# Kernel tuning notes

Hardware: AMD Instinct MI355X
Metric: run time of the kernel (lower is better)

## Reference

```python
import jax, jax.numpy as jnp
import numpy as np

N_NODES = 100000
N_EDGES = 3200000
IN_DIM, HID_DIM, OUT_DIM = 8, 64, 112

def _glorot(key, fan_in, fan_out):
    lim = jnp.sqrt(6.0 / (fan_in + fan_out))
    return jax.random.uniform(key, (fan_in, fan_out), jnp.float32, -lim, lim)

def setup_inputs() -> dict:
    key = jax.random.key(0)
    ks = jax.random.split(key, 8)
    x = jax.random.normal(ks[0], (N_NODES, IN_DIM), jnp.float32)
    edge_index = jax.random.randint(ks[1], (2, N_EDGES), 0, N_NODES, jnp.int64 if jax.config.read('jax_enable_x64') else jnp.int32)
    return {
        'x': x,
        'edge_index': edge_index,
        'W1': _glorot(ks[2], IN_DIM, HID_DIM),  'b1': jnp.zeros((HID_DIM,), jnp.float32),
        'W2': _glorot(ks[3], HID_DIM, HID_DIM), 'b2': jnp.zeros((HID_DIM,), jnp.float32),
        'W3': _glorot(ks[4], HID_DIM, OUT_DIM), 'b3': jnp.zeros((OUT_DIM,), jnp.float32),
    }

def _gcn_conv(x, src, dst, W, b, n):
    # PyG GCNConv: add self-loops, symmetric normalization, x @ W, scatter-add, + bias
    h = x @ W                                   # [N, F_out]
    loop = jnp.arange(n, dtype=src.dtype)
    s = jnp.concatenate([src, loop])            # source (j)
    d = jnp.concatenate([dst, loop])            # target (i)
    deg = jax.ops.segment_sum(jnp.ones_like(d, dtype=h.dtype), d, num_segments=n)
    dinv = jnp.where(deg > 0, jax.lax.rsqrt(deg), 0.0)
    norm = dinv[s] * dinv[d]                    # [E+N]
    msg = h[s] * norm[:, None]                  # gather + scale, [E+N, F_out]
    out = jax.ops.segment_sum(msg, d, num_segments=n)
    return out + b

def reference(x, edge_index, W1, b1, W2, b2, W3, b3):
    # eval mode: dropout is identity
    n = x.shape[0]
    src, dst = edge_index[0], edge_index[1]
    h = jax.nn.relu(_gcn_conv(x, src, dst, W1, b1, n))
    h = jax.nn.relu(_gcn_conv(h, src, dst, W2, b2, n))
    return _gcn_conv(h, src, dst, W3, b3, n)
```

## Files before the change

### kernel.cpp

```cpp
#include <hip/hip_runtime.h>
#include <hip/hip_fp16.h>


#define NNODES 100000
#define NEDGES 3200000
#define BW     128
#define NB     ((NNODES + BW - 1) / BW)
#define NSUB   8
#define SUBCAP 768
#define CAP    (NSUB * SUBCAP)
#define PAD    16
#define SLOTCAP 72
#define TILE   4096
#define EPT    (TILE / 256)
#define NFB    ((NEDGES + TILE - 1) / TILE)

typedef unsigned long long u64;


__global__ void bcur_init_kernel(int* __restrict__ bcur) {
    int i = blockIdx.x * blockDim.x + threadIdx.x;
    if (i < NB * NSUB) {
        int b  = i / NSUB;
        int xc = i % NSUB;
        bcur[i * PAD] = b * CAP + xc * SUBCAP;
    }
}

__global__ __launch_bounds__(256) void bfill_kernel(
        const int* __restrict__ src, const int* __restrict__ dst,
        int* __restrict__ bcur, u64* __restrict__ tmp) {
    __shared__ int cnt[NB];
    __shared__ int gbase[NB];
    int xc = blockIdx.x & (NSUB - 1);
    int e0 = blockIdx.x * TILE;

    for (int t = threadIdx.x; t < NB; t += 256) cnt[t] = 0;
    __syncthreads();

    u64 pk[EPT];
    int bb[EPT];
    int loff[EPT];
#pragma unroll
    for (int j = 0; j < EPT; ++j) {
        int e = e0 + j * 256 + threadIdx.x;
        if (e < NEDGES) {
            int d = dst[e];
            int s = src[e];
            bb[j] = d >> 7;
            pk[j] = ((u64)(unsigned)d << 32) | (unsigned)s;
            loff[j] = atomicAdd(&cnt[bb[j]], 1);
        } else {
            bb[j] = -1;
        }
    }
    __syncthreads();

    for (int b = threadIdx.x; b < NB; b += 256) {
        int c = cnt[b];
        gbase[b] = c ? atomicAdd(&bcur[(b * NSUB + xc) * PAD], c) : 0;
    }
    __syncthreads();

#pragma unroll
    for (int j = 0; j < EPT; ++j) {
        if (bb[j] >= 0) {
            int b = bb[j];
            int p = gbase[b] + loff[j];
            int sb = b * CAP + xc * SUBCAP;
            if ((unsigned)(p - sb) < (unsigned)SUBCAP)
                tmp[p] = pk[j];
        }
    }
}

__global__ void place_kernel(const u64* __restrict__ tmp, const int* __restrict__ bcur,
                             int* __restrict__ csr_src, int* __restrict__ rend,
                             float* __restrict__ dinv) {
    __shared__ int cur[BW];
    int b  = blockIdx.x;
    int lo = b * BW;

    for (int t = threadIdx.x; t < BW; t += blockDim.x)
        cur[t] = (lo + t) * SLOTCAP;
    __syncthreads();
#pragma unroll
    for (int xc = 0; xc < NSUB; ++xc) {
        int sb = b * CAP + xc * SUBCAP;
        int se = bcur[(b * NSUB + xc) * PAD];
        if (se > sb + SUBCAP) se = sb + SUBCAP;
        for (int k = sb + threadIdx.x; k < se; k += blockDim.x) {
            u64 pk = __builtin_nontemporal_load(&tmp[k]);
            int d = (int)(pk >> 32) - lo;
            int s = (int)(pk & 0xffffffffu);
            if ((unsigned)d < (unsigned)BW) {
                int pos = atomicAdd(&cur[d], 1);
                if (pos - (lo + d) * SLOTCAP < SLOTCAP)
                    csr_src[pos] = s;
            }
        }
    }
    __syncthreads();
    for (int t = threadIdx.x; t < BW; t += blockDim.x) {
        int i = lo + t;
        if (i < NNODES) {
            int deg = cur[t] - i * SLOTCAP;
            if (deg > SLOTCAP) deg = SLOTCAP;
            rend[i] = i * SLOTCAP + deg;
            dinv[i] = rsqrtf((float)deg + 1.0f);
        }
    }
}


__global__ void prescale_kernel(const float* __restrict__ x, const float* __restrict__ dinv,
                                float* __restrict__ xs) {
    int idx = blockIdx.x * blockDim.x + threadIdx.x;
    if (idx >= NNODES * 2) return;
    float di = dinv[idx >> 1];
    float4 v = ((const float4*)x)[idx];
    v.x *= di; v.y *= di; v.z *= di; v.w *= di;
    ((float4*)xs)[idx] = v;
}

#define ACC4(A, V) { A.x += V.x; A.y += V.y; A.z += V.z; A.w += V.w; }

template<int F>
__global__ void gather_kernel(const float* __restrict__ hs, const int* __restrict__ rend,
                              const int* __restrict__ csr_src, float* __restrict__ agg) {
    constexpr int NQ = F / 4;
    int idx = blockIdx.x * blockDim.x + threadIdx.x;
    if (idx >= NNODES * NQ) return;
    int i = idx / NQ;
    int q = idx % NQ;

    const float4* t4 = (const float4*)hs;
    float4 a0 = t4[i * NQ + q];
    float4 a1 = make_float4(0.f, 0.f, 0.f, 0.f), a2 = a1, a3 = a1;
    int beg = i * SLOTCAP, end = rend[i];
    int k = beg;
    for (; k + 4 <= end; k += 4) {
        int s0 = __builtin_nontemporal_load(&csr_src[k + 0]);
        int s1 = __builtin_nontemporal_load(&csr_src[k + 1]);
        int s2 = __builtin_nontemporal_load(&csr_src[k + 2]);
        int s3 = __builtin_nontemporal_load(&csr_src[k + 3]);
        float4 v0 = t4[s0 * NQ + q];
        float4 v1 = t4[s1 * NQ + q];
        float4 v2 = t4[s2 * NQ + q];
        float4 v3 = t4[s3 * NQ + q];
        ACC4(a0, v0) ACC4(a1, v1) ACC4(a2, v2) ACC4(a3, v3)
    }
    for (; k < end; ++k) {
        float4 v = t4[csr_src[k] * NQ + q];
        ACC4(a0, v)
    }
    ACC4(a0, a1) ACC4(a2, a3) ACC4(a0, a2)
    ((float4*)agg)[i * NQ + q] = a0;
}

#define H8_ACC(RAW, X0, X1) {                                            \
        const __half2* hp_ = (const __half2*)&(RAW);                     \
        float2 f0_ = __half22float2(hp_[0]);                             \
        float2 f1_ = __half22float2(hp_[1]);                             \
        float2 f2_ = __half22float2(hp_[2]);                             \
        float2 f3_ = __half22float2(hp_[3]);                             \
        X0.x += f0_.x; X0.y += f0_.y; X0.z += f1_.x; X0.w += f1_.y;      \
        X1.x += f2_.x; X1.y += f2_.y; X1.z += f3_.x; X1.w += f3_.y; }

__global__ void gather64h_kernel(const __half* __restrict__ hs, const int* __restrict__ rend,
                                 const int* __restrict__ csr_src, float* __restrict__ agg) {
    int idx = blockIdx.x * blockDim.x + threadIdx.x;
    if (idx >= NNODES * 8) return;
    int i = idx >> 3;
    int q = idx & 7;

    const float4* h4 = (const float4*)hs;
    float4 a0 = make_float4(0.f, 0.f, 0.f, 0.f), a1 = a0, b0 = a0, b1 = a0;

    float4 self = h4[(size_t)i * 8 + q];
    H8_ACC(self, a0, a1)

    int beg = i * SLOTCAP, end = rend[i];
    int k = beg;
    for (; k + 4 <= end; k += 4) {
        int s0 = __builtin_nontemporal_load(&csr_src[k + 0]);
        int s1 = __builtin_nontemporal_load(&csr_src[k + 1]);
        int s2 = __builtin_nontemporal_load(&csr_src[k + 2]);
        int s3 = __builtin_nontemporal_load(&csr_src[k + 3]);
        float4 r0 = h4[(size_t)s0 * 8 + q];
        float4 r1 = h4[(size_t)s1 * 8 + q];
        float4 r2 = h4[(size_t)s2 * 8 + q];
        float4 r3 = h4[(size_t)s3 * 8 + q];
        H8_ACC(r0, a0, a1) H8_ACC(r1, b0, b1) H8_ACC(r2, a0, a1) H8_ACC(r3, b0, b1)
    }
    for (; k < end; ++k) {
        float4 r = h4[(size_t)csr_src[k] * 8 + q];
        H8_ACC(r, a0, a1)
    }
    ACC4(a0, b0) ACC4(a1, b1)

    float4* o4 = (float4*)(agg + (size_t)i * 64 + q * 8);
    o4[0] = a0;
    o4[1] = a1;
}

template<int FIN, int FOUT, bool RELU, bool SCALE, bool OUTH>
__global__ __launch_bounds__(256) void transform_kernel(
        const float* __restrict__ agg, const float* __restrict__ dinv,
        const float* __restrict__ W, const float* __restrict__ b,
        void* __restrict__ outp) {
    __shared__ float Ws[FIN * FOUT];
    __shared__ float bs[FOUT];
    for (int t = threadIdx.x; t < FIN * FOUT; t += 256) Ws[t] = W[t];
    for (int t = threadIdx.x; t < FOUT; t += 256) bs[t] = b[t];
    __syncthreads();

    int i = blockIdx.x * 256 + threadIdx.x;
    if (i >= NNODES) return;

    const float4* row4 = (const float4*)(agg + (size_t)i * FIN);
    float di = dinv[i];

    constexpr int NC = FOUT / 16;
    for (int c = 0; c < NC; ++c) {
        float4 a0 = make_float4(0.f, 0.f, 0.f, 0.f), a1 = a0, a2 = a0, a3 = a0;
        const float* wbase = Ws + c * 16;
#define FMA16(RV, KK) { const float4* wq = (const float4*)(wbase + (KK) * FOUT);     \
        float4 w0 = wq[0], w1 = wq[1], w2 = wq[2], w3 = wq[3];                       \
        a0.x += (RV)*w0.x; a0.y += (RV)*w0.y; a0.z += (RV)*w0.z; a0.w += (RV)*w0.w;  \
        a1.x += (RV)*w1.x; a1.y += (RV)*w1.y; a1.z += (RV)*w1.z; a1.w += (RV)*w1.w;  \
        a2.x += (RV)*w2.x; a2.y += (RV)*w2.y; a2.z += (RV)*w2.z; a2.w += (RV)*w2.w;  \
        a3.x += (RV)*w3.x; a3.y += (RV)*w3.y; a3.z += (RV)*w3.z; a3.w += (RV)*w3.w; }
#pragma unroll
        for (int k4 = 0; k4 < FIN / 4; ++k4) {
            float4 rv = row4[k4];
            FMA16(rv.x, 4 * k4 + 0)
            FMA16(rv.y, 4 * k4 + 1)
            FMA16(rv.z, 4 * k4 + 2)
            FMA16(rv.w, 4 * k4 + 3)
        }
#undef FMA16
        const float4* bq = (const float4*)(bs + c * 16);
        float4 b0 = bq[0], b1 = bq[1], b2 = bq[2], b3 = bq[3];
#define POST(A, B) { A.x = A.x * di + B.x; A.y = A.y * di + B.y;                     \
        A.z = A.z * di + B.z; A.w = A.w * di + B.w;                                  \
        if (RELU) { A.x = fmaxf(A.x, 0.f); A.y = fmaxf(A.y, 0.f);                    \
                    A.z = fmaxf(A.z, 0.f); A.w = fmaxf(A.w, 0.f); }                  \
        if (SCALE) { A.x *= di; A.y *= di; A.z *= di; A.w *= di; } }
        POST(a0, b0) POST(a1, b1) POST(a2, b2) POST(a3, b3)
#undef POST
        if (OUTH) {
            __half* hout = (__half*)outp + (size_t)i * FOUT;
            union { float4 f4; __half2 h2[4]; } u0, u1;
            u0.h2[0] = __floats2half2_rn(a0.x, a0.y);
            u0.h2[1] = __floats2half2_rn(a0.z, a0.w);
            u0.h2[2] = __floats2half2_rn(a1.x, a1.y);
            u0.h2[3] = __floats2half2_rn(a1.z, a1.w);
            u1.h2[0] = __floats2half2_rn(a2.x, a2.y);
            u1.h2[1] = __floats2half2_rn(a2.z, a2.w);
            u1.h2[2] = __floats2half2_rn(a3.x, a3.y);
            u1.h2[3] = __floats2half2_rn(a3.z, a3.w);
            ((float4*)hout)[c * 2 + 0] = u0.f4;
            ((float4*)hout)[c * 2 + 1] = u1.f4;
        } else {
            float4* out4 = (float4*)((float*)outp + (size_t)i * FOUT);
            out4[c * 4 + 0] = a0;
            out4[c * 4 + 1] = a1;
            out4[c * 4 + 2] = a2;
            out4[c * 4 + 3] = a3;
        }
    }
}

extern "C" void kernel_launch(void* const* d_in, const int* in_sizes, int n_in,
                              void* d_out, int out_size, void* d_ws, size_t ws_size,
                              hipStream_t stream) {
    const float* x  = (const float*)d_in[0];
    const int*   ei = (const int*)d_in[1];
    const float* W1 = (const float*)d_in[2];
    const float* b1 = (const float*)d_in[3];
    const float* W2 = (const float*)d_in[4];
    const float* b2 = (const float*)d_in[5];
    const float* W3 = (const float*)d_in[6];
    const float* b3 = (const float*)d_in[7];

    const int* src = ei;
    const int* dst = ei + NEDGES;

    float* out = (float*)d_out;

    char* w = (char*)d_ws;
    int*   bcur    = (int*)w;                 w += NB * NSUB * PAD * 4;
    int*   rend    = (int*)w;                 w += ((NNODES + 3) / 4) * 16;
    float* dinv    = (float*)w;               w += ((NNODES + 3) / 4) * 16;
    int*   csr_src = (int*)w;                 w += (size_t)NNODES * SLOTCAP * 4;
    float* xs      = (float*)w;               w += (size_t)NNODES * 8 * 4;
    float* aggX    = (float*)w;               w += (size_t)NNODES * 8 * 4;
    char*  big     = w;                       w += (size_t)NB * CAP * 8;
    u64*    tmp   = (u64*)big;
    float*  bufG  = (float*)big;
    __half* bufHh = (__half*)(big + (size_t)NNODES * 64 * 4);

    const int B = 256;
    int gC   = (NB * NSUB + B - 1) / B;
    int gN2  = (NNODES * 2 + B - 1) / B;
    int gT   = (NNODES + 255) / 256;
    int gG8  = (NNODES * 2 + B - 1) / B;
    int gG64 = (NNODES * 8 + B - 1) / B;

    bcur_init_kernel<<<gC, B, 0, stream>>>(bcur);
    bfill_kernel <<<NFB, 256, 0, stream>>>(src, dst, bcur, tmp);
    place_kernel <<<NB, B, 0, stream>>>(tmp, bcur, csr_src, rend, dinv);

    prescale_kernel<<<gN2, B, 0, stream>>>(x, dinv, xs);
    gather_kernel<8><<<gG8, B, 0, stream>>>(xs, rend, csr_src, aggX);
    transform_kernel<8, 64, true, true, true><<<gT, 256, 0, stream>>>(aggX, dinv, W1, b1, bufHh);

    gather64h_kernel<<<gG64, B, 0, stream>>>(bufHh, rend, csr_src, bufG);
    transform_kernel<64, 64, true, true, true><<<gT, 256, 0, stream>>>(bufG, dinv, W2, b2, bufHh);

    gather64h_kernel<<<gG64, B, 0, stream>>>(bufHh, rend, csr_src, bufG);
    transform_kernel<64, 112, false, false, false><<<gT, 256, 0, stream>>>(bufG, dinv, W3, b3, out);
}
```

Baseline: 343.6 us.

## Fuse 64-wide neighbor gather with dense transform and enlarge bucket-fill tiles

```diff
diff --git a/kernel.cpp b/kernel.cpp
--- a/kernel.cpp
+++ b/kernel.cpp
@@ -11,8 +11,9 @@
 #define CAP    (NSUB * SUBCAP)
 #define PAD    16
 #define SLOTCAP 72
-#define TILE   4096
-#define EPT    (TILE / 256)
+#define BFT    512
+#define TILE   8192
+#define EPT    (TILE / BFT)
 #define NFB    ((NEDGES + TILE - 1) / TILE)
 
 typedef unsigned long long u64;
@@ -27,7 +28,7 @@
     }
 }
 
-__global__ __launch_bounds__(256) void bfill_kernel(
+__global__ __launch_bounds__(BFT) void bfill_kernel(
         const int* __restrict__ src, const int* __restrict__ dst,
         int* __restrict__ bcur, u64* __restrict__ tmp) {
     __shared__ int cnt[NB];
@@ -35,7 +36,7 @@
     int xc = blockIdx.x & (NSUB - 1);
     int e0 = blockIdx.x * TILE;
 
-    for (int t = threadIdx.x; t < NB; t += 256) cnt[t] = 0;
+    for (int t = threadIdx.x; t < NB; t += BFT) cnt[t] = 0;
     __syncthreads();
 
     u64 pk[EPT];
@@ -43,7 +44,7 @@
     int loff[EPT];
 #pragma unroll
     for (int j = 0; j < EPT; ++j) {
-        int e = e0 + j * 256 + threadIdx.x;
+        int e = e0 + j * BFT + threadIdx.x;
         if (e < NEDGES) {
             int d = dst[e];
             int s = src[e];
@@ -56,7 +57,7 @@
     }
     __syncthreads();
 
-    for (int b = threadIdx.x; b < NB; b += 256) {
+    for (int b = threadIdx.x; b < NB; b += BFT) {
         int c = cnt[b];
         gbase[b] = c ? atomicAdd(&bcur[(b * NSUB + xc) * PAD], c) : 0;
     }
@@ -158,57 +159,11 @@
     ((float4*)agg)[i * NQ + q] = a0;
 }
 
-#define H8_ACC(RAW, X0, X1) {                                            \
-        const __half2* hp_ = (const __half2*)&(RAW);                     \
-        float2 f0_ = __half22float2(hp_[0]);                             \
-        float2 f1_ = __half22float2(hp_[1]);                             \
-        float2 f2_ = __half22float2(hp_[2]);                             \
-        float2 f3_ = __half22float2(hp_[3]);                             \
-        X0.x += f0_.x; X0.y += f0_.y; X0.z += f1_.x; X0.w += f1_.y;      \
-        X1.x += f2_.x; X1.y += f2_.y; X1.z += f3_.x; X1.w += f3_.y; }
-
-__global__ void gather64h_kernel(const __half* __restrict__ hs, const int* __restrict__ rend,
-                                 const int* __restrict__ csr_src, float* __restrict__ agg) {
-    int idx = blockIdx.x * blockDim.x + threadIdx.x;
-    if (idx >= NNODES * 8) return;
-    int i = idx >> 3;
-    int q = idx & 7;
-
-    const float4* h4 = (const float4*)hs;
-    float4 a0 = make_float4(0.f, 0.f, 0.f, 0.f), a1 = a0, b0 = a0, b1 = a0;
-
-    float4 self = h4[(size_t)i * 8 + q];
-    H8_ACC(self, a0, a1)
-
-    int beg = i * SLOTCAP, end = rend[i];
-    int k = beg;
-    for (; k + 4 <= end; k += 4) {
-        int s0 = __builtin_nontemporal_load(&csr_src[k + 0]);
-        int s1 = __builtin_nontemporal_load(&csr_src[k + 1]);
-        int s2 = __builtin_nontemporal_load(&csr_src[k + 2]);
-        int s3 = __builtin_nontemporal_load(&csr_src[k + 3]);
-        float4 r0 = h4[(size_t)s0 * 8 + q];
-        float4 r1 = h4[(size_t)s1 * 8 + q];
-        float4 r2 = h4[(size_t)s2 * 8 + q];
-        float4 r3 = h4[(size_t)s3 * 8 + q];
-        H8_ACC(r0, a0, a1) H8_ACC(r1, b0, b1) H8_ACC(r2, a0, a1) H8_ACC(r3, b0, b1)
-    }
-    for (; k < end; ++k) {
-        float4 r = h4[(size_t)csr_src[k] * 8 + q];
-        H8_ACC(r, a0, a1)
-    }
-    ACC4(a0, b0) ACC4(a1, b1)
-
-    float4* o4 = (float4*)(agg + (size_t)i * 64 + q * 8);
-    o4[0] = a0;
-    o4[1] = a1;
-}
-
-template<int FIN, int FOUT, bool RELU, bool SCALE, bool OUTH>
+template<int FIN, int FOUT>
 __global__ __launch_bounds__(256) void transform_kernel(
         const float* __restrict__ agg, const float* __restrict__ dinv,
         const float* __restrict__ W, const float* __restrict__ b,
-        void* __restrict__ outp) {
+        __half* __restrict__ outp) {
     __shared__ float Ws[FIN * FOUT];
     __shared__ float bs[FOUT];
     for (int t = threadIdx.x; t < FIN * FOUT; t += 256) Ws[t] = W[t];
@@ -242,32 +197,147 @@
 #undef FMA16
         const float4* bq = (const float4*)(bs + c * 16);
         float4 b0 = bq[0], b1 = bq[1], b2 = bq[2], b3 = bq[3];
-#define POST(A, B) { A.x = A.x * di + B.x; A.y = A.y * di + B.y;                     \
-        A.z = A.z * di + B.z; A.w = A.w * di + B.w;                                  \
-        if (RELU) { A.x = fmaxf(A.x, 0.f); A.y = fmaxf(A.y, 0.f);                    \
-                    A.z = fmaxf(A.z, 0.f); A.w = fmaxf(A.w, 0.f); }                  \
-        if (SCALE) { A.x *= di; A.y *= di; A.z *= di; A.w *= di; } }
+#define POST(A, B) { A.x = fmaxf(A.x * di + B.x, 0.f) * di;                          \
+        A.y = fmaxf(A.y * di + B.y, 0.f) * di;                                       \
+        A.z = fmaxf(A.z * di + B.z, 0.f) * di;                                       \
+        A.w = fmaxf(A.w * di + B.w, 0.f) * di; }
         POST(a0, b0) POST(a1, b1) POST(a2, b2) POST(a3, b3)
 #undef POST
+        __half* hout = outp + (size_t)i * FOUT;
+        union { float4 f4; __half2 h2[4]; } u0, u1;
+        u0.h2[0] = __floats2half2_rn(a0.x, a0.y);
+        u0.h2[1] = __floats2half2_rn(a0.z, a0.w);
+        u0.h2[2] = __floats2half2_rn(a1.x, a1.y);
+        u0.h2[3] = __floats2half2_rn(a1.z, a1.w);
+        u1.h2[0] = __floats2half2_rn(a2.x, a2.y);
+        u1.h2[1] = __floats2half2_rn(a2.z, a2.w);
+        u1.h2[2] = __floats2half2_rn(a3.x, a3.y);
+        u1.h2[3] = __floats2half2_rn(a3.z, a3.w);
+        ((float4*)hout)[c * 2 + 0] = u0.f4;
+        ((float4*)hout)[c * 2 + 1] = u1.f4;
+    }
+}
+
+
+#define H8_TO(RAW, X0, X1) {                                             \
+        const __half2* hp_ = (const __half2*)&(RAW);                     \
+        float2 f0_ = __half22float2(hp_[0]);                             \
+        float2 f1_ = __half22float2(hp_[1]);                             \
+        float2 f2_ = __half22float2(hp_[2]);                             \
+        float2 f3_ = __half22float2(hp_[3]);                             \
+        X0.x += f0_.x; X0.y += f0_.y; X0.z += f1_.x; X0.w += f1_.y;      \
+        X1.x += f2_.x; X1.y += f2_.y; X1.z += f3_.x; X1.w += f3_.y; }
+
+#define ROWE(KK) ((KK & 3) == 0 ? A[KK >> 2].x : (KK & 3) == 1 ? A[KK >> 2].y \
+                 : (KK & 3) == 2 ? A[KK >> 2].z : A[KK >> 2].w)
+
+template<int FOUT, bool RELU, bool SCALE, bool OUTH>
+__global__ __launch_bounds__(256) void fused64_kernel(
+        const __half* __restrict__ hs, const int* __restrict__ rend,
+        const int* __restrict__ csr_src, const float* __restrict__ dinv,
+        const float* __restrict__ W, const float* __restrict__ b,
+        void* __restrict__ outp) {
+    constexpr int CH  = (FOUT % 32 == 0) ? 32 : 28;
+    constexpr int NCH = FOUT / CH;
+    constexpr int NQ  = CH / 4;
+    __shared__ float Ws[64 * FOUT];
+    __shared__ float bs[FOUT];
+    for (int t = threadIdx.x; t < 64 * FOUT; t += 256) Ws[t] = W[t];
+    for (int t = threadIdx.x; t < FOUT; t += 256) bs[t] = b[t];
+    __syncthreads();
+
+    int idx = blockIdx.x * 256 + threadIdx.x;
+    if (idx >= NNODES * 2) return;
+    int i = idx >> 1;
+    int h = idx & 1;
+
+    const float4* h4 = (const float4*)hs;
+    size_t qb = (size_t)i * 8 + h * 4;
+
+    float4 A[8];
+#pragma unroll
+    for (int j = 0; j < 8; ++j) A[j] = make_float4(0.f, 0.f, 0.f, 0.f);
+    {
+        float4 s0 = h4[qb + 0], s1 = h4[qb + 1], s2 = h4[qb + 2], s3 = h4[qb + 3];
+        H8_TO(s0, A[0], A[1]) H8_TO(s1, A[2], A[3])
+        H8_TO(s2, A[4], A[5]) H8_TO(s3, A[6], A[7])
+    }
+    int beg = i * SLOTCAP, end = rend[i];
+    int k = beg;
+    for (; k + 2 <= end; k += 2) {
+        int n0 = __builtin_nontemporal_load(&csr_src[k + 0]);
+        int n1 = __builtin_nontemporal_load(&csr_src[k + 1]);
+        size_t q0 = (size_t)n0 * 8 + h * 4;
+        size_t q1 = (size_t)n1 * 8 + h * 4;
+        float4 r0 = h4[q0 + 0], r1 = h4[q0 + 1], r2 = h4[q0 + 2], r3 = h4[q0 + 3];
+        float4 t0 = h4[q1 + 0], t1 = h4[q1 + 1], t2 = h4[q1 + 2], t3 = h4[q1 + 3];
+        H8_TO(r0, A[0], A[1]) H8_TO(r1, A[2], A[3])
+        H8_TO(r2, A[4], A[5]) H8_TO(r3, A[6], A[7])
+        H8_TO(t0, A[0], A[1]) H8_TO(t1, A[2], A[3])
+        H8_TO(t2, A[4], A[5]) H8_TO(t3, A[6], A[7])
+    }
+    for (; k < end; ++k) {
+        int n0 = __builtin_nontemporal_load(&csr_src[k]);
+        size_t q0 = (size_t)n0 * 8 + h * 4;
+        float4 r0 = h4[q0 + 0], r1 = h4[q0 + 1], r2 = h4[q0 + 2], r3 = h4[q0 + 3];
+        H8_TO(r0, A[0], A[1]) H8_TO(r1, A[2], A[3])
+        H8_TO(r2, A[4], A[5]) H8_TO(r3, A[6], A[7])
+    }
+
+    float di = dinv[i];
+    int kb = h * 32;
+
+    for (int c = 0; c < NCH; ++c) {
+        float4 C[NQ];
+#pragma unroll
+        for (int j = 0; j < NQ; ++j) C[j] = make_float4(0.f, 0.f, 0.f, 0.f);
+#pragma unroll
+        for (int kk = 0; kk < 32; ++kk) {
+            float rv = ROWE(kk);
+            const float4* wq = (const float4*)(Ws + (kb + kk) * FOUT + c * CH);
+#pragma unroll
+            for (int j = 0; j < NQ; ++j) {
+                C[j].x += rv * wq[j].x; C[j].y += rv * wq[j].y;
+                C[j].z += rv * wq[j].z; C[j].w += rv * wq[j].w;
+            }
+        }
+#pragma unroll
+        for (int j = 0; j < NQ; ++j) {
+            C[j].x += __shfl_xor(C[j].x, 1);
+            C[j].y += __shfl_xor(C[j].y, 1);
+            C[j].z += __shfl_xor(C[j].z, 1);
+            C[j].w += __shfl_xor(C[j].w, 1);
+        }
+        const float4* bq = (const float4*)(bs + c * CH);
+#pragma unroll
+        for (int j = 0; j < NQ; ++j) {
+            float4 bb = bq[j];
+            C[j].x = C[j].x * di + bb.x; C[j].y = C[j].y * di + bb.y;
+            C[j].z = C[j].z * di + bb.z; C[j].w = C[j].w * di + bb.w;
+            if (RELU) {
+                C[j].x = fmaxf(C[j].x, 0.f); C[j].y = fmaxf(C[j].y, 0.f);
+                C[j].z = fmaxf(C[j].z, 0.f); C[j].w = fmaxf(C[j].w, 0.f);
+            }
+            if (SCALE) { C[j].x *= di; C[j].y *= di; C[j].z *= di; C[j].w *= di; }
+        }
         if (OUTH) {
-            __half* hout = (__half*)outp + (size_t)i * FOUT;
-            union { float4 f4; __half2 h2[4]; } u0, u1;
-            u0.h2[0] = __floats2half2_rn(a0.x, a0.y);
-            u0.h2[1] = __floats2half2_rn(a0.z, a0.w);
-            u0.h2[2] = __floats2half2_rn(a1.x, a1.y);
-            u0.h2[3] = __floats2half2_rn(a1.z, a1.w);
-            u1.h2[0] = __floats2half2_rn(a2.x, a2.y);
-            u1.h2[1] = __floats2half2_rn(a2.z, a2.w);
-            u1.h2[2] = __floats2half2_rn(a3.x, a3.y);
-            u1.h2[3] = __floats2half2_rn(a3.z, a3.w);
-            ((float4*)hout)[c * 2 + 0] = u0.f4;
-            ((float4*)hout)[c * 2 + 1] = u1.f4;
+            __half* hrow = (__half*)outp + (size_t)i * FOUT + c * CH;
+#pragma unroll
+            for (int p = 0; p < NQ / 2; ++p) {
+                if ((p & 1) == h) {
+                    union { float4 f4; __half2 h2[4]; } u;
+                    u.h2[0] = __floats2half2_rn(C[2 * p].x, C[2 * p].y);
+                    u.h2[1] = __floats2half2_rn(C[2 * p].z, C[2 * p].w);
+                    u.h2[2] = __floats2half2_rn(C[2 * p + 1].x, C[2 * p + 1].y);
+                    u.h2[3] = __floats2half2_rn(C[2 * p + 1].z, C[2 * p + 1].w);
+                    ((float4*)hrow)[p] = u.f4;
+                }
+            }
         } else {
-            float4* out4 = (float4*)((float*)outp + (size_t)i * FOUT);
-            out4[c * 4 + 0] = a0;
-            out4[c * 4 + 1] = a1;
-            out4[c * 4 + 2] = a2;
-            out4[c * 4 + 3] = a3;
+            float* orow = (float*)outp + (size_t)i * FOUT + c * CH;
+#pragma unroll
+            for (int j = 0; j < NQ; ++j)
+                if ((j & 1) == h) ((float4*)orow)[j] = C[j];
         }
     }
 }
@@ -297,28 +367,28 @@
     float* xs      = (float*)w;               w += (size_t)NNODES * 8 * 4;
     float* aggX    = (float*)w;               w += (size_t)NNODES * 8 * 4;
     char*  big     = w;                       w += (size_t)NB * CAP * 8;
-    u64*    tmp   = (u64*)big;
-    float*  bufG  = (float*)big;
-    __half* bufHh = (__half*)(big + (size_t)NNODES * 64 * 4);
+    u64*    tmp    = (u64*)big;
+    __half* stateA = (__half*)big;
+    __half* stateB = (__half*)(big + (size_t)NNODES * 64 * 2);
 
     const int B = 256;
     int gC   = (NB * NSUB + B - 1) / B;
     int gN2  = (NNODES * 2 + B - 1) / B;
     int gT   = (NNODES + 255) / 256;
     int gG8  = (NNODES * 2 + B - 1) / B;
-    int gG64 = (NNODES * 8 + B - 1) / B;
+    int gF   = (NNODES * 2 + 255) / 256;
 
     bcur_init_kernel<<<gC, B, 0, stream>>>(bcur);
-    bfill_kernel <<<NFB, 256, 0, stream>>>(src, dst, bcur, tmp);
+    bfill_kernel <<<NFB, BFT, 0, stream>>>(src, dst, bcur, tmp);
     place_kernel <<<NB, B, 0, stream>>>(tmp, bcur, csr_src, rend, dinv);
 
     prescale_kernel<<<gN2, B, 0, stream>>>(x, dinv, xs);
     gather_kernel<8><<<gG8, B, 0, stream>>>(xs, rend, csr_src, aggX);
-    transform_kernel<8, 64, true, true, true><<<gT, 256, 0, stream>>>(aggX, dinv, W1, b1, bufHh);
-
-    gather64h_kernel<<<gG64, B, 0, stream>>>(bufHh, rend, csr_src, bufG);
-    transform_kernel<64, 64, true, true, true><<<gT, 256, 0, stream>>>(bufG, dinv, W2, b2, bufHh);
-
-    gather64h_kernel<<<gG64, B, 0, stream>>>(bufHh, rend, csr_src, bufG);
-    transform_kernel<64, 112, false, false, false><<<gT, 256, 0, stream>>>(bufG, dinv, W3, b3, out);
-}
+    transform_kernel<8, 64><<<gT, 256, 0, stream>>>(aggX, dinv, W1, b1, stateA);
+
+    fused64_kernel<64, true, true, true><<<gF, 256, 0, stream>>>(
+        stateA, rend, csr_src, dinv, W2, b2, stateB);
+
+    fused64_kernel<112, false, false, false><<<gF, 256, 0, stream>>>(
+        stateB, rend, csr_src, dinv, W3, b3, out);
+}
```

Result: slower. 391.6 us (+14.0%).

## Pack bucketed edges into 32-bit words and enlarge bucket-fill tiles

Applied to the files above, without the earlier changes.

```diff
diff --git a/kernel.cpp b/kernel.cpp
--- a/kernel.cpp
+++ b/kernel.cpp
@@ -11,11 +11,12 @@
 #define CAP    (NSUB * SUBCAP)
 #define PAD    16
 #define SLOTCAP 72
-#define TILE   4096
-#define EPT    (TILE / 256)
+#define BFT    512
+#define TILE   8192
+#define EPT    (TILE / BFT)
 #define NFB    ((NEDGES + TILE - 1) / TILE)
 
-typedef unsigned long long u64;
+typedef unsigned int u32;
 
 
 __global__ void bcur_init_kernel(int* __restrict__ bcur) {
@@ -27,28 +28,28 @@
     }
 }
 
-__global__ __launch_bounds__(256) void bfill_kernel(
+__global__ __launch_bounds__(BFT) void bfill_kernel(
         const int* __restrict__ src, const int* __restrict__ dst,
-        int* __restrict__ bcur, u64* __restrict__ tmp) {
+        int* __restrict__ bcur, u32* __restrict__ tmp) {
     __shared__ int cnt[NB];
     __shared__ int gbase[NB];
     int xc = blockIdx.x & (NSUB - 1);
     int e0 = blockIdx.x * TILE;
 
-    for (int t = threadIdx.x; t < NB; t += 256) cnt[t] = 0;
-    __syncthreads();
-
-    u64 pk[EPT];
+    for (int t = threadIdx.x; t < NB; t += BFT) cnt[t] = 0;
+    __syncthreads();
+
+    u32 pk[EPT];
     int bb[EPT];
     int loff[EPT];
 #pragma unroll
     for (int j = 0; j < EPT; ++j) {
-        int e = e0 + j * 256 + threadIdx.x;
+        int e = e0 + j * BFT + threadIdx.x;
         if (e < NEDGES) {
             int d = dst[e];
             int s = src[e];
             bb[j] = d >> 7;
-            pk[j] = ((u64)(unsigned)d << 32) | (unsigned)s;
+            pk[j] = ((u32)(d & 127) << 25) | (u32)s;
             loff[j] = atomicAdd(&cnt[bb[j]], 1);
         } else {
             bb[j] = -1;
@@ -56,7 +57,7 @@
     }
     __syncthreads();
 
-    for (int b = threadIdx.x; b < NB; b += 256) {
+    for (int b = threadIdx.x; b < NB; b += BFT) {
         int c = cnt[b];
         gbase[b] = c ? atomicAdd(&bcur[(b * NSUB + xc) * PAD], c) : 0;
     }
@@ -74,7 +75,7 @@
     }
 }
 
-__global__ void place_kernel(const u64* __restrict__ tmp, const int* __restrict__ bcur,
+__global__ void place_kernel(const u32* __restrict__ tmp, const int* __restrict__ bcur,
                              int* __restrict__ csr_src, int* __restrict__ rend,
                              float* __restrict__ dinv) {
     __shared__ int cur[BW];
@@ -90,14 +91,12 @@
         int se = bcur[(b * NSUB + xc) * PAD];
         if (se > sb + SUBCAP) se = sb + SUBCAP;
         for (int k = sb + threadIdx.x; k < se; k += blockDim.x) {
-            u64 pk = __builtin_nontemporal_load(&tmp[k]);
-            int d = (int)(pk >> 32) - lo;
-            int s = (int)(pk & 0xffffffffu);
-            if ((unsigned)d < (unsigned)BW) {
-                int pos = atomicAdd(&cur[d], 1);
-                if (pos - (lo + d) * SLOTCAP < SLOTCAP)
-                    csr_src[pos] = s;
-            }
+            u32 pk = __builtin_nontemporal_load(&tmp[k]);
+            int d = (int)(pk >> 25);
+            int s = (int)(pk & 0x1FFFFFFu);
+            int pos = atomicAdd(&cur[d], 1);
+            if (pos - (lo + d) * SLOTCAP < SLOTCAP)
+                csr_src[pos] = s;
         }
     }
     __syncthreads();
@@ -296,8 +295,9 @@
     int*   csr_src = (int*)w;                 w += (size_t)NNODES * SLOTCAP * 4;
     float* xs      = (float*)w;               w += (size_t)NNODES * 8 * 4;
     float* aggX    = (float*)w;               w += (size_t)NNODES * 8 * 4;
-    char*  big     = w;                       w += (size_t)NB * CAP * 8;
-    u64*    tmp   = (u64*)big;
+    char*  big     = w;                       w += (size_t)NNODES * 64 * 4 +
+                                                   (size_t)NNODES * 64 * 2;
+    u32*    tmp   = (u32*)big;
     float*  bufG  = (float*)big;
     __half* bufHh = (__half*)(big + (size_t)NNODES * 64 * 4);
 
@@ -309,7 +309,7 @@
     int gG64 = (NNODES * 8 + B - 1) / B;
 
     bcur_init_kernel<<<gC, B, 0, stream>>>(bcur);
-    bfill_kernel <<<NFB, 256, 0, stream>>>(src, dst, bcur, tmp);
+    bfill_kernel <<<NFB, BFT, 0, stream>>>(src, dst, bcur, tmp);
     place_kernel <<<NB, B, 0, stream>>>(tmp, bcur, csr_src, rend, dinv);
 
     prescale_kernel<<<gN2, B, 0, stream>>>(x, dinv, xs);
```

New measurement: 313.9 us. 8.6% less time.
